# Kernel optimization log

Hardware: AMD Instinct MI355X
Metric: run time of the kernel (lower is better)

The kernel has to match this reference:

```python
import jax, jax.numpy as jnp
import numpy as np

EPSILON = 1e-15
LOG2 = 0.6931471805599453
N_VARS = 4096
BATCH = 512
OUT_SIZES = [16384, 8192, 4096, 2048]
FANINS = [4, 2, 4, 2]


def log1mexp(x):
    # accurate log(1 - exp(x)) for x < 0
    return jnp.where(x > -LOG2,
                     jnp.log(-jnp.expm1(x)),
                     jnp.log1p(-jnp.exp(x)))


def encode_input(pos):
    # rows: [-inf, 0, pos0, neg0, pos1, neg1, ...]
    neg = log1mexp(pos)
    inter = jnp.stack([pos, neg], axis=1).reshape(2 * pos.shape[0], pos.shape[1])
    head = jnp.stack([jnp.full(pos.shape[1:], -jnp.inf, pos.dtype),
                      jnp.zeros(pos.shape[1:], pos.dtype)])
    return jnp.concatenate([head, inter], axis=0)


def product_layer(x, ptrs, seg, n_out):
    return jax.ops.segment_sum(x[ptrs], seg, num_segments=n_out)


def sum_layer(x, ptrs, seg, n_out):
    g = x[ptrs]
    a = jax.lax.stop_gradient(jax.ops.segment_max(g, seg, num_segments=n_out))
    s = jax.ops.segment_sum(jnp.exp(g - a[seg]), seg, num_segments=n_out)
    return jnp.log(s + EPSILON) + a


def setup_inputs() -> dict:
    rng = np.random.default_rng(0)
    # log-probabilities in (-inf, 0): pos = log(u), u in (0,1)
    u = rng.uniform(1e-4, 1.0 - 1e-4, size=(N_VARS, BATCH)).astype(np.float32)
    x = jnp.asarray(np.log(u))

    inputs = {"x": x}
    prev_size = 2 * N_VARS + 2
    for i, (n_out, fanin) in enumerate(zip(OUT_SIZES, FANINS)):
        n_edges = n_out * fanin
        lo = 1 if i == 0 else 0  # avoid the -inf constant row at layer 0
        ptrs = rng.integers(lo, prev_size, size=n_edges).astype(np.int64)
        seg = np.repeat(np.arange(n_out, dtype=np.int64), fanin)
        inputs[f"ptrs{i}"] = jnp.asarray(ptrs)
        inputs[f"seg{i}"] = jnp.asarray(seg)
        prev_size = n_out
    return inputs


def reference(x, ptrs0, seg0, ptrs1, seg1, ptrs2, seg2, ptrs3, seg3):
    h = encode_input(x)
    ptrs = [ptrs0, ptrs1, ptrs2, ptrs3]
    segs = [seg0, seg1, seg2, seg3]
    for i, n_out in enumerate(OUT_SIZES):
        if i % 2 == 0:
            h = product_layer(h, ptrs[i], segs[i], n_out)
        else:
            h = sum_layer(h, ptrs[i], segs[i], n_out)
    return h
```

## Files before the change

kernel.cpp:

```cpp
#include <hip/hip_runtime.h>
#include <math.h>

#define BATCH    512
#define N_VARS   4096
#define H_ROWS   (2 * N_VARS + 2)
#define N_OUT1   8192
#define N_OUT3   2048
#define TPB      1024
#define SMEM_BYTES (H_ROWS * sizeof(float2))

__device__ __forceinline__ float log1mexp_fast(float x) {
    return __logf(1.0f - __expf(x));
}

__device__ __forceinline__ float2 lse2_fast2(float2 a, float2 b) {
    float2 r;
    r.x = fmaxf(a.x, b.x) + __logf(1.0f + __expf(-fabsf(a.x - b.x)));
    r.y = fmaxf(a.y, b.y) + __logf(1.0f + __expf(-fabsf(a.y - b.y)));
    return r;
}

#define TDIM    32
#define NTRANS  ((BATCH / TDIM) * (N_VARS / TDIM))
#define NTAB    ((N_OUT1 + N_OUT3) / 256)
__global__ void prep_kernel(const float* __restrict__ x,
                            float* __restrict__ xT,
                            const int* __restrict__ p0,
                            const int* __restrict__ p1,
                            const int* __restrict__ p2,
                            const int* __restrict__ p3,
                            int4* __restrict__ tabB,
                            int4* __restrict__ tabC) {
    __shared__ float tile[TDIM][TDIM + 1];
    int blk = blockIdx.x;
    int tx = threadIdx.x, ty = threadIdx.y;
    if (blk < NTRANS) {
        int cb = (blk % (BATCH / TDIM)) * TDIM;
        int rb = (blk / (BATCH / TDIM)) * TDIM;
#pragma unroll
        for (int j = 0; j < TDIM; j += 8)
            tile[ty + j][tx] = x[(size_t)(rb + ty + j) * BATCH + cb + tx];
        __syncthreads();
#pragma unroll
        for (int j = 0; j < TDIM; j += 8)
            xT[(size_t)(cb + ty + j) * N_VARS + rb + tx] = tile[tx][ty + j];
    } else {
        int o = (blk - NTRANS) * 256 + ty * TDIM + tx;
        if (o < N_OUT1) {
            int2 pp = ((const int2*)p1)[o];
            tabB[2 * o]     = ((const int4*)p0)[pp.x];
            tabB[2 * o + 1] = ((const int4*)p0)[pp.y];
        } else {
            int oc = o - N_OUT1;
            int2 pp = ((const int2*)p3)[oc];
            tabC[2 * oc]     = ((const int4*)p2)[pp.x];
            tabC[2 * oc + 1] = ((const int4*)p2)[pp.y];
        }
    }
}

__global__ void __launch_bounds__(TPB, 4)
fused_spn_kernel(const float* __restrict__ xT,
                 const int4* __restrict__ tabB,
                 const int4* __restrict__ tabC,
                 float* __restrict__ out) {
    extern __shared__ float2 buf[];
    const int bp = blockIdx.x;
    const int t = threadIdx.x;

    if (t == 0) {
        buf[0] = make_float2(-INFINITY, -INFINITY);
        buf[1] = make_float2(0.f, 0.f);
    }
    {
        float4 pa = ((const float4*)(xT + (size_t)(2 * bp)     * N_VARS))[t];
        float4 pb = ((const float4*)(xT + (size_t)(2 * bp + 1) * N_VARS))[t];
        int base = 8 * t + 2;
        buf[base + 0] = make_float2(pa.x, pb.x);
        buf[base + 1] = make_float2(log1mexp_fast(pa.x), log1mexp_fast(pb.x));
        buf[base + 2] = make_float2(pa.y, pb.y);
        buf[base + 3] = make_float2(log1mexp_fast(pa.y), log1mexp_fast(pb.y));
        buf[base + 4] = make_float2(pa.z, pb.z);
        buf[base + 5] = make_float2(log1mexp_fast(pa.z), log1mexp_fast(pb.z));
        buf[base + 6] = make_float2(pa.w, pb.w);
        buf[base + 7] = make_float2(log1mexp_fast(pa.w), log1mexp_fast(pb.w));
    }
    __syncthreads();

    float2 r1[N_OUT1 / TPB];
#pragma unroll
    for (int c = 0; c < N_OUT1 / TPB; c += 4) {
        int4 qa[4], qb[4];
#pragma unroll
        for (int k = 0; k < 4; ++k) {
            int o = t + (c + k) * TPB;
            qa[k] = tabB[2 * o];
            qb[k] = tabB[2 * o + 1];
        }
#pragma unroll
        for (int k = 0; k < 4; ++k) {
            float2 va0 = buf[qa[k].x], va1 = buf[qa[k].y];
            float2 va2 = buf[qa[k].z], va3 = buf[qa[k].w];
            float2 vb0 = buf[qb[k].x], vb1 = buf[qb[k].y];
            float2 vb2 = buf[qb[k].z], vb3 = buf[qb[k].w];
            float2 ga = make_float2(va0.x + va1.x + va2.x + va3.x,
                                    va0.y + va1.y + va2.y + va3.y);
            float2 gb = make_float2(vb0.x + vb1.x + vb2.x + vb3.x,
                                    vb0.y + vb1.y + vb2.y + vb3.y);
            r1[c + k] = lse2_fast2(ga, gb);
        }
    }
    __syncthreads();
#pragma unroll
    for (int k = 0; k < N_OUT1 / TPB; ++k)
        buf[t + k * TPB] = r1[k];
    __syncthreads();

    {
        int4 qa[2], qb[2];
#pragma unroll
        for (int k = 0; k < 2; ++k) {
            int o = t + k * TPB;
            qa[k] = tabC[2 * o];
            qb[k] = tabC[2 * o + 1];
        }
#pragma unroll
        for (int k = 0; k < 2; ++k) {
            int o = t + k * TPB;
            float2 va0 = buf[qa[k].x], va1 = buf[qa[k].y];
            float2 va2 = buf[qa[k].z], va3 = buf[qa[k].w];
            float2 vb0 = buf[qb[k].x], vb1 = buf[qb[k].y];
            float2 vb2 = buf[qb[k].z], vb3 = buf[qb[k].w];
            float2 ga = make_float2(va0.x + va1.x + va2.x + va3.x,
                                    va0.y + va1.y + va2.y + va3.y);
            float2 gb = make_float2(vb0.x + vb1.x + vb2.x + vb3.x,
                                    vb0.y + vb1.y + vb2.y + vb3.y);
            ((float2*)(out + (size_t)o * BATCH))[bp] = lse2_fast2(ga, gb);
        }
    }
}

extern "C" void kernel_launch(void* const* d_in, const int* in_sizes, int n_in,
                              void* d_out, int out_size, void* d_ws, size_t ws_size,
                              hipStream_t stream) {
    const float* x     = (const float*)d_in[0];
    const int*   ptrs0 = (const int*)d_in[1];
    const int*   ptrs1 = (const int*)d_in[3];
    const int*   ptrs2 = (const int*)d_in[5];
    const int*   ptrs3 = (const int*)d_in[7];
    float* out = (float*)d_out;

    float* xT  = (float*)d_ws;
    int4*  tabB = (int4*)(xT + (size_t)N_VARS * BATCH);
    int4*  tabC = tabB + 2 * N_OUT1;

    hipFuncSetAttribute((const void*)fused_spn_kernel,
                        hipFuncAttributeMaxDynamicSharedMemorySize, SMEM_BYTES);

    prep_kernel<<<NTRANS + NTAB, dim3(32, 8), 0, stream>>>(
        x, xT, ptrs0, ptrs1, ptrs2, ptrs3, tabB, tabC);

    fused_spn_kernel<<<BATCH / 2, TPB, SMEM_BYTES, stream>>>(xT, tabB, tabC, out);
}
```

Baseline: 89.41 us.

## Encode input layer as fp16 pairs in prep kernel and split smem buffers

```diff
diff --git a/kernel.cpp b/kernel.cpp
--- a/kernel.cpp
+++ b/kernel.cpp
@@ -1,4 +1,5 @@
 #include <hip/hip_runtime.h>
+#include <hip/hip_fp16.h>
 #include <math.h>
 
 #define BATCH    512
@@ -7,7 +8,12 @@
 #define N_OUT1   8192
 #define N_OUT3   2048
 #define TPB      1024
-#define SMEM_BYTES (H_ROWS * sizeof(float2))
+
+#define S_U2       4100
+#define ENC_BYTES  (S_U2 * 8)
+#define ENC_WS_BYTES ((size_t)(BATCH / 2) * ENC_BYTES)
+#define R1_BYTES   (N_OUT1 * 8)
+#define SMEM_BYTES (ENC_BYTES + R1_BYTES)
 
 __device__ __forceinline__ float log1mexp_fast(float x) {
     return __logf(1.0f - __expf(x));
@@ -20,11 +26,27 @@
     return r;
 }
 
+__device__ __forceinline__ unsigned int h2u(__half2 h) {
+    union { __half2 h; unsigned int u; } v; v.h = h; return v.u;
+}
+
+__device__ __forceinline__ float2 gsum_h(const __half2* __restrict__ enc, int4 q) {
+    __half2 v0 = enc[q.x], v1 = enc[q.y], v2 = enc[q.z], v3 = enc[q.w];
+    __half2 s01 = __hadd2(v0, v1), s23 = __hadd2(v2, v3);
+    float2 f01 = __half22float2(s01), f23 = __half22float2(s23);
+    return make_float2(f01.x + f23.x, f01.y + f23.y);
+}
+
+__device__ __forceinline__ float2 gsum_f(const float2* __restrict__ rb, int4 q) {
+    float2 v0 = rb[q.x], v1 = rb[q.y], v2 = rb[q.z], v3 = rb[q.w];
+    return make_float2(v0.x + v1.x + v2.x + v3.x, v0.y + v1.y + v2.y + v3.y);
+}
+
 #define TDIM    32
 #define NTRANS  ((BATCH / TDIM) * (N_VARS / TDIM))
 #define NTAB    ((N_OUT1 + N_OUT3) / 256)
 __global__ void prep_kernel(const float* __restrict__ x,
-                            float* __restrict__ xT,
+                            uint2* __restrict__ encE,
                             const int* __restrict__ p0,
                             const int* __restrict__ p1,
                             const int* __restrict__ p2,
@@ -41,9 +63,21 @@
         for (int j = 0; j < TDIM; j += 8)
             tile[ty + j][tx] = x[(size_t)(rb + ty + j) * BATCH + cb + tx];
         __syncthreads();
+        int tid = ty * TDIM + tx;
 #pragma unroll
-        for (int j = 0; j < TDIM; j += 8)
-            xT[(size_t)(cb + ty + j) * N_VARS + rb + tx] = tile[tx][ty + j];
+        for (int k = 0; k < 2; ++k) {
+            int q = tid + k * 256;
+            int vl = q & 31;
+            int pl = q >> 5;
+            float a = tile[vl][2 * pl];
+            float b = tile[vl][2 * pl + 1];
+            uint2 val;
+            val.x = h2u(__floats2half2_rn(a, b));
+            val.y = h2u(__floats2half2_rn(log1mexp_fast(a), log1mexp_fast(b)));
+            encE[(size_t)(cb / 2 + pl) * S_U2 + 1 + rb + vl] = val;
+        }
+        if (rb == 0 && tid < 16)
+            encE[(size_t)(cb / 2 + tid) * S_U2] = make_uint2(0xFC00FC00u, 0u);
     } else {
         int o = (blk - NTRANS) * 256 + ty * TDIM + tx;
         if (o < N_OUT1) {
@@ -60,83 +94,50 @@
 }
 
 __global__ void __launch_bounds__(TPB, 4)
-fused_spn_kernel(const float* __restrict__ xT,
+fused_spn_kernel(const uint2* __restrict__ encE,
                  const int4* __restrict__ tabB,
                  const int4* __restrict__ tabC,
                  float* __restrict__ out) {
-    extern __shared__ float2 buf[];
+    extern __shared__ char smem[];
+    const __half2* enc = (const __half2*)smem;
+    float2* r1b = (float2*)(smem + ENC_BYTES);
     const int bp = blockIdx.x;
-    const int t = threadIdx.x;
+    const int t  = threadIdx.x;
 
-    if (t == 0) {
-        buf[0] = make_float2(-INFINITY, -INFINITY);
-        buf[1] = make_float2(0.f, 0.f);
-    }
+    const uint2* src = encE + (size_t)bp * S_U2;
+    uint2 e0 = src[t], e1 = src[t + 1024], e2 = src[t + 2048], e3 = src[t + 3072];
+    int4 a0A = tabB[2 * t],          b0A = tabB[2 * t + 1];
+    int4 a1A = tabB[2 * (t + 1024)], b1A = tabB[2 * (t + 1024) + 1];
     {
-        float4 pa = ((const float4*)(xT + (size_t)(2 * bp)     * N_VARS))[t];
-        float4 pb = ((const float4*)(xT + (size_t)(2 * bp + 1) * N_VARS))[t];
-        int base = 8 * t + 2;
-        buf[base + 0] = make_float2(pa.x, pb.x);
-        buf[base + 1] = make_float2(log1mexp_fast(pa.x), log1mexp_fast(pb.x));
-        buf[base + 2] = make_float2(pa.y, pb.y);
-        buf[base + 3] = make_float2(log1mexp_fast(pa.y), log1mexp_fast(pb.y));
-        buf[base + 4] = make_float2(pa.z, pb.z);
-        buf[base + 5] = make_float2(log1mexp_fast(pa.z), log1mexp_fast(pb.z));
-        buf[base + 6] = make_float2(pa.w, pb.w);
-        buf[base + 7] = make_float2(log1mexp_fast(pa.w), log1mexp_fast(pb.w));
+        uint2* lu2 = (uint2*)smem;
+        lu2[t] = e0; lu2[t + 1024] = e1; lu2[t + 2048] = e2; lu2[t + 3072] = e3;
+        if (t == 0) lu2[4096] = src[4096];
     }
     __syncthreads();
 
-    float2 r1[N_OUT1 / TPB];
-#pragma unroll
-    for (int c = 0; c < N_OUT1 / TPB; c += 4) {
-        int4 qa[4], qb[4];
-#pragma unroll
-        for (int k = 0; k < 4; ++k) {
-            int o = t + (c + k) * TPB;
-            qa[k] = tabB[2 * o];
-            qb[k] = tabB[2 * o + 1];
-        }
-#pragma unroll
-        for (int k = 0; k < 4; ++k) {
-            float2 va0 = buf[qa[k].x], va1 = buf[qa[k].y];
-            float2 va2 = buf[qa[k].z], va3 = buf[qa[k].w];
-            float2 vb0 = buf[qb[k].x], vb1 = buf[qb[k].y];
-            float2 vb2 = buf[qb[k].z], vb3 = buf[qb[k].w];
-            float2 ga = make_float2(va0.x + va1.x + va2.x + va3.x,
-                                    va0.y + va1.y + va2.y + va3.y);
-            float2 gb = make_float2(vb0.x + vb1.x + vb2.x + vb3.x,
-                                    vb0.y + vb1.y + vb2.y + vb3.y);
-            r1[c + k] = lse2_fast2(ga, gb);
-        }
-    }
-    __syncthreads();
-#pragma unroll
-    for (int k = 0; k < N_OUT1 / TPB; ++k)
-        buf[t + k * TPB] = r1[k];
+    int4 a0B = tabB[2 * (t + 2048)], b0B = tabB[2 * (t + 2048) + 1];
+    int4 a1B = tabB[2 * (t + 3072)], b1B = tabB[2 * (t + 3072) + 1];
+    r1b[t]        = lse2_fast2(gsum_h(enc, a0A), gsum_h(enc, b0A));
+    r1b[t + 1024] = lse2_fast2(gsum_h(enc, a1A), gsum_h(enc, b1A));
+    a0A = tabB[2 * (t + 4096)]; b0A = tabB[2 * (t + 4096) + 1];
+    a1A = tabB[2 * (t + 5120)]; b1A = tabB[2 * (t + 5120) + 1];
+    r1b[t + 2048] = lse2_fast2(gsum_h(enc, a0B), gsum_h(enc, b0B));
+    r1b[t + 3072] = lse2_fast2(gsum_h(enc, a1B), gsum_h(enc, b1B));
+    a0B = tabB[2 * (t + 6144)]; b0B = tabB[2 * (t + 6144) + 1];
+    a1B = tabB[2 * (t + 7168)]; b1B = tabB[2 * (t + 7168) + 1];
+    r1b[t + 4096] = lse2_fast2(gsum_h(enc, a0A), gsum_h(enc, b0A));
+    r1b[t + 5120] = lse2_fast2(gsum_h(enc, a1A), gsum_h(enc, b1A));
+    int4 ca0 = tabC[2 * t],          cb0 = tabC[2 * t + 1];
+    int4 ca1 = tabC[2 * (t + 1024)], cb1 = tabC[2 * (t + 1024) + 1];
+    r1b[t + 6144] = lse2_fast2(gsum_h(enc, a0B), gsum_h(enc, b0B));
+    r1b[t + 7168] = lse2_fast2(gsum_h(enc, a1B), gsum_h(enc, b1B));
     __syncthreads();
 
     {
-        int4 qa[2], qb[2];
-#pragma unroll
-        for (int k = 0; k < 2; ++k) {
-            int o = t + k * TPB;
-            qa[k] = tabC[2 * o];
-            qb[k] = tabC[2 * o + 1];
-        }
-#pragma unroll
-        for (int k = 0; k < 2; ++k) {
-            int o = t + k * TPB;
-            float2 va0 = buf[qa[k].x], va1 = buf[qa[k].y];
-            float2 va2 = buf[qa[k].z], va3 = buf[qa[k].w];
-            float2 vb0 = buf[qb[k].x], vb1 = buf[qb[k].y];
-            float2 vb2 = buf[qb[k].z], vb3 = buf[qb[k].w];
-            float2 ga = make_float2(va0.x + va1.x + va2.x + va3.x,
-                                    va0.y + va1.y + va2.y + va3.y);
-            float2 gb = make_float2(vb0.x + vb1.x + vb2.x + vb3.x,
-                                    vb0.y + vb1.y + vb2.y + vb3.y);
-            ((float2*)(out + (size_t)o * BATCH))[bp] = lse2_fast2(ga, gb);
-        }
+        float2 ga = gsum_f(r1b, ca0), gb = gsum_f(r1b, cb0);
+        ((float2*)(out + (size_t)t * BATCH))[bp] = lse2_fast2(ga, gb);
+        float2 ga1 = gsum_f(r1b, ca1), gb1 = gsum_f(r1b, cb1);
+        ((float2*)(out + (size_t)(t + 1024) * BATCH))[bp] = lse2_fast2(ga1, gb1);
     }
 }
 
@@ -150,15 +151,15 @@
     const int*   ptrs3 = (const int*)d_in[7];
     float* out = (float*)d_out;
 
-    float* xT  = (float*)d_ws;
-    int4*  tabB = (int4*)(xT + (size_t)N_VARS * BATCH);
+    uint2* encE = (uint2*)d_ws;
+    int4*  tabB = (int4*)((char*)d_ws + ENC_WS_BYTES);
     int4*  tabC = tabB + 2 * N_OUT1;
 
     hipFuncSetAttribute((const void*)fused_spn_kernel,
                         hipFuncAttributeMaxDynamicSharedMemorySize, SMEM_BYTES);
 
     prep_kernel<<<NTRANS + NTAB, dim3(32, 8), 0, stream>>>(
-        x, xT, ptrs0, ptrs1, ptrs2, ptrs3, tabB, tabC);
+        x, encE, ptrs0, ptrs1, ptrs2, ptrs3, tabB, tabC);
 
-    fused_spn_kernel<<<BATCH / 2, TPB, SMEM_BYTES, stream>>>(xT, tabB, tabC, out);
+    fused_spn_kernel<<<BATCH / 2, TPB, SMEM_BYTES, stream>>>(encE, tabB, tabC, out);
 }
```

Result: no change. 88.81 us (-0.7%).
